# Kernel tuning notes

Hardware: AMD Instinct MI355X
Metric: run time of the kernel (lower is better)

Reference implementation:

```python
import jax, jax.numpy as jnp
import numpy as np

DELTA = 2.0

def _pearson(x, y):
    vx = x - jnp.mean(x)
    vy = y - jnp.mean(y)
    return jnp.sum(vx * vy) / (jnp.sqrt(jnp.sum(vx ** 2)) * jnp.sqrt(jnp.sum(vy ** 2)))

def setup_inputs() -> dict:
    key = jax.random.key(0)
    k1, k2 = jax.random.split(key)
    n = 4000000
    output = jax.random.normal(k1, (n, 6), dtype=jnp.float32)
    label = jax.random.normal(k2, (n, 1), dtype=jnp.float32)
    return {"output": output, "label": label}

def reference(output, label):
    # output: [n, 6] = [q0, q1, q2, q3, q4, q]; label: [n, 1]
    target = label[:, 0]  # [n]

    # Pearson correlation of each of the 6 prediction columns vs label
    plcc = [_pearson(output[:, i], target) for i in range(6)]

    # Per-sample weighted pseudo-Huber loss (vectorized over batch)
    diff = output - label                      # [n, 6] (pred - target)
    huber = DELTA ** 2 * (jnp.sqrt(1.0 + (diff / DELTA) ** 2) - 1.0)  # [n, 6]
    alpha_head = 0.2 * jnp.tanh(diff[:, :5]) ** 2                     # [n, 5]
    alpha = jnp.concatenate([alpha_head, jnp.ones_like(diff[:, 5:6])], axis=1)  # [n, 6]
    loss_old = jnp.mean(jnp.sum(huber * alpha, axis=1))

    p0, p1, p2, p3, p4, p5 = plcc
    s = 5.0 - p0 - p1 - p2 - p3 - p4
    plcc_pen = ((1 - p0) ** 2 + (1 - p1) ** 2 + (1 - p2) ** 2 + (1 - p3) ** 2 + (1 - p4) ** 2) / s
    loss = loss_old + plcc_pen + (1.0 - p5)
    return loss
```

## Files before the change

kernel.cpp:

```cpp
#include <hip/hip_runtime.h>
#include <math.h>

static constexpr int BLOCK = 256;
static constexpr int NACC  = 21;

__device__ __forceinline__ float fast_tanh_sq(float d) {
    float e = __expf(2.0f * d);
    float r = __builtin_amdgcn_rcpf(e + 1.0f);
    float t = 1.0f - 2.0f * r;
    return t * t;
}

__device__ __forceinline__ void row_accum(float acc[NACC], const float x[6], float y) {
    acc[18] += y;
    acc[19] += y * y;
    float rowh = 0.0f;
#pragma unroll
    for (int c = 0; c < 6; ++c) {
        const float xv = x[c];
        acc[c]      += xv;
        acc[6 + c]  += xv * xv;
        acc[12 + c] += xv * y;
        const float d   = xv - y;
        const float hub = 4.0f * (__builtin_amdgcn_sqrtf(1.0f + 0.25f * d * d) - 1.0f);
        const float al  = (c < 5) ? (0.2f * fast_tanh_sq(d)) : 1.0f;
        rowh += hub * al;
    }
    acc[20] += rowh;
}

__global__ __launch_bounds__(BLOCK) void huber_partial_kernel(
    const float* __restrict__ out6,
    const float* __restrict__ lab,
    float* __restrict__ part,
    int n)
{
    float acc[NACC];
#pragma unroll
    for (int k = 0; k < NACC; ++k) acc[k] = 0.0f;

    const int npairs = n >> 1;
    const int tid    = blockIdx.x * blockDim.x + threadIdx.x;
    const int stride = gridDim.x * blockDim.x;

    for (int p = tid; p < npairs; p += stride) {
        const float4* base = reinterpret_cast<const float4*>(out6 + (size_t)p * 12);
        const float4 a = base[0];
        const float4 b = base[1];
        const float4 c = base[2];
        const float2 y2 = *reinterpret_cast<const float2*>(lab + (size_t)p * 2);

        const float r0[6] = {a.x, a.y, a.z, a.w, b.x, b.y};
        const float r1[6] = {b.z, b.w, c.x, c.y, c.z, c.w};
        row_accum(acc, r0, y2.x);
        row_accum(acc, r1, y2.y);
    }

    if ((n & 1) && tid == 0) {
        const size_t row = (size_t)n - 1;
        float xr[6];
#pragma unroll
        for (int c = 0; c < 6; ++c) xr[c] = out6[row * 6 + c];
        row_accum(acc, xr, lab[row]);
    }

#pragma unroll
    for (int k = 0; k < NACC; ++k) {
        float v = acc[k];
#pragma unroll
        for (int off = 32; off > 0; off >>= 1)
            v += __shfl_down(v, off, 64);
        acc[k] = v;
    }

    __shared__ float red[BLOCK / 64][NACC];
    const int wave = threadIdx.x >> 6;
    const int lane = threadIdx.x & 63;
    if (lane == 0) {
#pragma unroll
        for (int k = 0; k < NACC; ++k) red[wave][k] = acc[k];
    }
    __syncthreads();
    if (threadIdx.x < NACC) {
        float s = 0.0f;
#pragma unroll
        for (int w = 0; w < BLOCK / 64; ++w) s += red[w][threadIdx.x];
        part[(size_t)blockIdx.x * NACC + threadIdx.x] = s;
    }
}

__global__ __launch_bounds__(64) void huber_final_kernel(
    const float* __restrict__ part, int nblocks, int n, float* __restrict__ out)
{
    double acc[NACC];
#pragma unroll
    for (int k = 0; k < NACC; ++k) acc[k] = 0.0;

    for (int b = threadIdx.x; b < nblocks; b += 64) {
        const float* p = part + (size_t)b * NACC;
#pragma unroll
        for (int k = 0; k < NACC; ++k) acc[k] += (double)p[k];
    }

#pragma unroll
    for (int k = 0; k < NACC; ++k) {
        double v = acc[k];
#pragma unroll
        for (int off = 32; off > 0; off >>= 1)
            v += __shfl_down(v, off, 64);
        acc[k] = v;
    }

    if (threadIdx.x == 0) {
        const double dn  = (double)n;
        const double Sy  = acc[18];
        const double Syy = acc[19];
        const double vary = Syy - Sy * Sy / dn;
        double pc[6];
#pragma unroll
        for (int c = 0; c < 6; ++c) {
            const double Sx  = acc[c];
            const double Sxx = acc[6 + c];
            const double Sxy = acc[12 + c];
            const double cov  = Sxy - Sx * Sy / dn;
            const double varx = Sxx - Sx * Sx / dn;
            pc[c] = cov / (sqrt(varx) * sqrt(vary));
        }
        const double loss_old = acc[20] / dn;
        const double s = 5.0 - pc[0] - pc[1] - pc[2] - pc[3] - pc[4];
        double pen = 0.0;
#pragma unroll
        for (int c = 0; c < 5; ++c) pen += (1.0 - pc[c]) * (1.0 - pc[c]);
        pen /= s;
        const double loss = loss_old + pen + (1.0 - pc[5]);
        out[0] = (float)loss;
    }
}

extern "C" void kernel_launch(void* const* d_in, const int* in_sizes, int n_in,
                              void* d_out, int out_size, void* d_ws, size_t ws_size,
                              hipStream_t stream) {
    const float* out6 = (const float*)d_in[0];
    const float* lab  = (const float*)d_in[1];
    float* out = (float*)d_out;
    const int n = in_sizes[1];

    int nblocks = 2048;
    const int maxb = (int)(ws_size / (NACC * sizeof(float)));
    if (nblocks > maxb) nblocks = maxb;
    int npairs = n >> 1;
    if (npairs < 1) npairs = 1;
    const int needed = (npairs + BLOCK - 1) / BLOCK;
    if (nblocks > needed) nblocks = needed;
    if (nblocks < 1) nblocks = 1;

    float* part = (float*)d_ws;
    hipLaunchKernelGGL(huber_partial_kernel, dim3(nblocks), dim3(BLOCK), 0, stream,
                       out6, lab, part, n);
    hipLaunchKernelGGL(huber_final_kernel, dim3(1), dim3(64), 0, stream,
                       part, nblocks, n, out);
}
```

Measured before the change: 176.6 us.

## Stage row tiles through LDS for coalesced loads and widen final reduction

The partial kernel now loads each 512-row tile of the output matrix into shared memory with fully coalesced float4 loads, one consecutive float4 per thread, instead of each thread reading three strided float4s. Threads then read their two rows from LDS. The goal is better global-memory coalescing for this bandwidth-bound reduction. It costs two barriers per tile and an LDS round trip. The final kernel also moves to 256 threads and reads padded partials with vectorized loads.

```diff
diff --git a/kernel.cpp b/kernel.cpp
--- a/kernel.cpp
+++ b/kernel.cpp
@@ -1,8 +1,12 @@
 #include <hip/hip_runtime.h>
 #include <math.h>
 
-static constexpr int BLOCK = 256;
-static constexpr int NACC  = 21;
+static constexpr int BLOCK     = 256;
+static constexpr int NACC      = 21;
+static constexpr int PSTRIDE   = 24;
+static constexpr int TILE_ROWS = 512;
+static constexpr int TILE_F4   = TILE_ROWS * 6 / 4;
+static constexpr int MAXBLOCKS = 2048;
 
 __device__ __forceinline__ float fast_tanh_sq(float d) {
     float e = __expf(2.0f * d);
@@ -35,28 +39,49 @@
     float* __restrict__ part,
     int n)
 {
+    __shared__ float4 tile[TILE_F4];
+    __shared__ float  red[BLOCK / 64][NACC];
+
     float acc[NACC];
 #pragma unroll
     for (int k = 0; k < NACC; ++k) acc[k] = 0.0f;
 
-    const int npairs = n >> 1;
-    const int tid    = blockIdx.x * blockDim.x + threadIdx.x;
-    const int stride = gridDim.x * blockDim.x;
-
-    for (int p = tid; p < npairs; p += stride) {
-        const float4* base = reinterpret_cast<const float4*>(out6 + (size_t)p * 12);
-        const float4 a = base[0];
-        const float4 b = base[1];
-        const float4 c = base[2];
-        const float2 y2 = *reinterpret_cast<const float2*>(lab + (size_t)p * 2);
-
-        const float r0[6] = {a.x, a.y, a.z, a.w, b.x, b.y};
-        const float r1[6] = {b.z, b.w, c.x, c.y, c.z, c.w};
-        row_accum(acc, r0, y2.x);
-        row_accum(acc, r1, y2.y);
-    }
-
-    if ((n & 1) && tid == 0) {
+    const int t  = threadIdx.x;
+    const int n2 = n & ~1;
+    const long long nf4 = ((long long)n2 * 6) >> 2;
+    const int ntiles = (n2 + TILE_ROWS - 1) / TILE_ROWS;
+    const float4* gsrc = reinterpret_cast<const float4*>(out6);
+
+    for (int tl = blockIdx.x; tl < ntiles; tl += gridDim.x) {
+        const long long basef4 = (long long)tl * TILE_F4;
+
+#pragma unroll
+        for (int k = 0; k < 3; ++k) {
+            const long long g = basef4 + k * BLOCK + t;
+            float4 v = make_float4(0.f, 0.f, 0.f, 0.f);
+            if (g < nf4) v = gsrc[g];
+            tile[k * BLOCK + t] = v;
+        }
+
+        const int r0 = tl * TILE_ROWS + 2 * t;
+        float2 y2 = make_float2(0.f, 0.f);
+        if (r0 + 1 < n2)
+            y2 = *reinterpret_cast<const float2*>(lab + r0);
+        __syncthreads();
+
+        if (r0 + 1 < n2) {
+            const float4 a = tile[3 * t + 0];
+            const float4 b = tile[3 * t + 1];
+            const float4 c = tile[3 * t + 2];
+            const float r0v[6] = {a.x, a.y, a.z, a.w, b.x, b.y};
+            const float r1v[6] = {b.z, b.w, c.x, c.y, c.z, c.w};
+            row_accum(acc, r0v, y2.x);
+            row_accum(acc, r1v, y2.y);
+        }
+        __syncthreads();
+    }
+
+    if ((n & 1) && blockIdx.x == 0 && t == 0) {
         const size_t row = (size_t)n - 1;
         float xr[6];
 #pragma unroll
@@ -73,60 +98,86 @@
         acc[k] = v;
     }
 
-    __shared__ float red[BLOCK / 64][NACC];
+    const int wave = t >> 6;
+    const int lane = t & 63;
+    if (lane == 0) {
+#pragma unroll
+        for (int k = 0; k < NACC; ++k) red[wave][k] = acc[k];
+    }
+    __syncthreads();
+    if (t < NACC) {
+        float s = 0.0f;
+#pragma unroll
+        for (int w = 0; w < BLOCK / 64; ++w) s += red[w][t];
+        part[(size_t)blockIdx.x * PSTRIDE + t] = s;
+    }
+}
+
+__global__ __launch_bounds__(BLOCK) void huber_final_kernel(
+    const float* __restrict__ part, int nblocks, int n, float* __restrict__ out)
+{
+    __shared__ double sred[BLOCK / 64][NACC];
+
+    double acc[NACC];
+#pragma unroll
+    for (int k = 0; k < NACC; ++k) acc[k] = 0.0;
+
+    for (int b = threadIdx.x; b < nblocks; b += BLOCK) {
+        const float* p = part + (size_t)b * PSTRIDE;
+        const float4* p4 = reinterpret_cast<const float4*>(p);
+#pragma unroll
+        for (int q = 0; q < 5; ++q) {
+            const float4 v = p4[q];
+            acc[q * 4 + 0] += (double)v.x;
+            acc[q * 4 + 1] += (double)v.y;
+            acc[q * 4 + 2] += (double)v.z;
+            acc[q * 4 + 3] += (double)v.w;
+        }
+        acc[20] += (double)p[20];
+    }
+
+#pragma unroll
+    for (int k = 0; k < NACC; ++k) {
+        double v = acc[k];
+#pragma unroll
+        for (int off = 32; off > 0; off >>= 1)
+            v += __shfl_down(v, off, 64);
+        acc[k] = v;
+    }
+
     const int wave = threadIdx.x >> 6;
     const int lane = threadIdx.x & 63;
     if (lane == 0) {
 #pragma unroll
-        for (int k = 0; k < NACC; ++k) red[wave][k] = acc[k];
+        for (int k = 0; k < NACC; ++k) sred[wave][k] = acc[k];
     }
     __syncthreads();
-    if (threadIdx.x < NACC) {
-        float s = 0.0f;
-#pragma unroll
-        for (int w = 0; w < BLOCK / 64; ++w) s += red[w][threadIdx.x];
-        part[(size_t)blockIdx.x * NACC + threadIdx.x] = s;
-    }
-}
-
-__global__ __launch_bounds__(64) void huber_final_kernel(
-    const float* __restrict__ part, int nblocks, int n, float* __restrict__ out)
-{
-    double acc[NACC];
-#pragma unroll
-    for (int k = 0; k < NACC; ++k) acc[k] = 0.0;
-
-    for (int b = threadIdx.x; b < nblocks; b += 64) {
-        const float* p = part + (size_t)b * NACC;
-#pragma unroll
-        for (int k = 0; k < NACC; ++k) acc[k] += (double)p[k];
-    }
-
-#pragma unroll
-    for (int k = 0; k < NACC; ++k) {
-        double v = acc[k];
-#pragma unroll
-        for (int off = 32; off > 0; off >>= 1)
-            v += __shfl_down(v, off, 64);
-        acc[k] = v;
-    }
 
     if (threadIdx.x == 0) {
+        double tot[NACC];
+#pragma unroll
+        for (int k = 0; k < NACC; ++k) {
+            double s = 0.0;
+#pragma unroll
+            for (int w = 0; w < BLOCK / 64; ++w) s += sred[w][k];
+            tot[k] = s;
+        }
+
         const double dn  = (double)n;
-        const double Sy  = acc[18];
-        const double Syy = acc[19];
+        const double Sy  = tot[18];
+        const double Syy = tot[19];
         const double vary = Syy - Sy * Sy / dn;
         double pc[6];
 #pragma unroll
         for (int c = 0; c < 6; ++c) {
-            const double Sx  = acc[c];
-            const double Sxx = acc[6 + c];
-            const double Sxy = acc[12 + c];
+            const double Sx  = tot[c];
+            const double Sxx = tot[6 + c];
+            const double Sxy = tot[12 + c];
             const double cov  = Sxy - Sx * Sy / dn;
             const double varx = Sxx - Sx * Sx / dn;
             pc[c] = cov / (sqrt(varx) * sqrt(vary));
         }
-        const double loss_old = acc[20] / dn;
+        const double loss_old = tot[20] / dn;
         const double s = 5.0 - pc[0] - pc[1] - pc[2] - pc[3] - pc[4];
         double pen = 0.0;
 #pragma unroll
@@ -145,18 +196,19 @@
     float* out = (float*)d_out;
     const int n = in_sizes[1];
 
-    int nblocks = 2048;
-    const int maxb = (int)(ws_size / (NACC * sizeof(float)));
-    if (nblocks > maxb) nblocks = maxb;
-    int npairs = n >> 1;
-    if (npairs < 1) npairs = 1;
-    const int needed = (npairs + BLOCK - 1) / BLOCK;
-    if (nblocks > needed) nblocks = needed;
-    if (nblocks < 1) nblocks = 1;
+    const int n2 = n & ~1;
+    int ntiles = (n2 + TILE_ROWS - 1) / TILE_ROWS;
+    if (ntiles < 1) ntiles = 1;
+
+    int nblocks = MAXBLOCKS;
+    const int maxb = (int)(ws_size / (PSTRIDE * sizeof(float)));
+    if (nblocks > maxb)   nblocks = maxb;
+    if (nblocks > ntiles) nblocks = ntiles;
+    if (nblocks < 1)      nblocks = 1;
 
     float* part = (float*)d_ws;
     hipLaunchKernelGGL(huber_partial_kernel, dim3(nblocks), dim3(BLOCK), 0, stream,
                        out6, lab, part, n);
-    hipLaunchKernelGGL(huber_final_kernel, dim3(1), dim3(64), 0, stream,
+    hipLaunchKernelGGL(huber_final_kernel, dim3(1), dim3(BLOCK), 0, stream,
                        part, nblocks, n, out);
 }
```

Result: faster. 165.5 us (-6.3%).
